# Kernel optimization log

Hardware: AMD Instinct MI355X
Metric: run time of the kernel (lower is better)

## Reference

```python
import jax, jax.numpy as jnp
import numpy as np

N, E, B, F, TLEN, NVOC, EMB, EPS = 131072, 1048576, 512, 78, 1000, 26, 128, 1e-5


def setup_inputs() -> dict:
    key = jax.random.key(0)
    ks = jax.random.split(key, 64)
    it = iter(range(64))

    def nrm(shp, s=0.05):
        return jax.random.normal(ks[next(it)], shp, jnp.float32) * s

    def bnp(c):  # row 0 = gamma, row 1 = beta (eval-mode BN, running stats = 0/1)
        return jnp.stack([1.0 + nrm((c,)), nrm((c,))])

    inp = {
        "x": jax.random.normal(ks[next(it)], (N, F), jnp.float32),
        "edge_index": jax.random.randint(ks[next(it)], (2, E), 0, N),
        "batch": jnp.repeat(jnp.arange(B), N // B),  # sorted graph ids, 256 nodes/graph
        "target": jax.random.randint(ks[next(it)], (B, TLEN), 0, NVOC),
        "W1": nrm((F, F)), "b1": nrm((F,)), "bn1": bnp(F), "Wp1": nrm((F, 1)), "bp1": nrm((1,)),
        "W2": nrm((F, F)), "b2": nrm((F,)), "bn2": bnp(F), "Wp2": nrm((F, 1)), "bp2": nrm((1,)),
        "W3": nrm((F, F)), "b3": nrm((F,)), "bn3": bnp(F), "Wp3": nrm((F, 1)), "bp3": nrm((1,)),
        "fcg1_W": nrm((2 * F, 128)), "fcg1_b": nrm((128,)), "bn4": bnp(128),
        "emb": nrm((NVOC, EMB), 1.0),
        "c1W": nrm((128, TLEN, 3)), "c1b": nrm((128,)), "bnx1": bnp(128),
        "c2W": nrm((64, 128, 3)), "c2b": nrm((64,)), "bnx2": bnp(64),
        "c3W": nrm((32, 64, 3)), "c3b": nrm((32,)), "bnx3": bnp(32),
        "fxt_W": nrm((32 * 128, 128)), "fxt_b": nrm((128,)), "bn6": bnp(128),
        "fc1W": nrm((256, 1024)), "fc1b": nrm((1024,)), "bn7": bnp(1024),
        "fc2W": nrm((1024, 512)), "fc2b": nrm((512,)), "bn8": bnp(512),
        "outW": nrm((512, 1)), "outb": nrm((1,)),
    }
    return inp


def _bn(h, p, axis=1):
    # eval-mode BatchNorm with running_mean=0, running_var=1
    sh = [1] * h.ndim
    sh[axis] = -1
    return h * (p[0] / jnp.sqrt(1.0 + EPS)).reshape(sh) + p[1].reshape(sh)


def reference(x, edge_index, batch, target, W1, b1, bn1, Wp1, bp1, W2, b2, bn2, Wp2, bp2,
              W3, b3, bn3, Wp3, bp3, fcg1_W, fcg1_b, bn4, emb, c1W, c1b, bnx1, c2W, c2b,
              bnx2, c3W, c3b, bnx3, fxt_W, fxt_b, bn6, fc1W, fc1b, bn7, fc2W, fc2b, bn8,
              outW, outb):
    src, dst = edge_index[0], edge_index[1]
    n = x.shape[0]

    # GCNConv with added self-loops and symmetric normalization
    deg = jax.ops.segment_sum(jnp.ones(src.shape[0], x.dtype), dst, num_segments=n) + 1.0
    dis = jax.lax.rsqrt(deg)                       # deg^{-1/2} including self-loop
    coef = (dis[src] * dis[dst])[:, None]          # [E,1]
    selfc = (dis * dis)[:, None]                   # [N,1]

    def gcn(h, W, b):
        h = h @ W
        agg = jax.ops.segment_sum(h[src] * coef, dst, num_segments=n)
        return agg + h * selfc + b

    def readout(h):
        mx = jax.ops.segment_max(h, batch, num_segments=B)
        cnt = jax.ops.segment_sum(jnp.ones(n, h.dtype), batch, num_segments=B)
        mean = jax.ops.segment_sum(h, batch, num_segments=B) / cnt[:, None]
        return jnp.concatenate([mx, mean], axis=1)  # [B, 2F]

    def block(h, W, b, bnp, Wp, bp):
        h = jax.nn.relu(_bn(gcn(h, W, b), bnp))
        # SAGPooling with ratio=1.0 keeps every node: x <- x * tanh(score)
        s = gcn(h, Wp, bp)[:, 0]
        return h * jnp.tanh(s)[:, None]

    h = block(x, W1, b1, bn1, Wp1, bp1); x1 = readout(h)
    h = block(h, W2, b2, bn2, Wp2, bp2); x2 = readout(h)
    h = block(h, W3, b3, bn3, Wp3, bp3); x3 = readout(h)
    g = jax.nn.relu(_bn((x1 + x2 + x3) @ fcg1_W + fcg1_b, bn4))

    # protein branch: embed [B,1000,128], conv1d over embed axis with 1000 in-channels
    def conv1d(h, W, b):
        o = jax.lax.conv_general_dilated(h, W, (1,), ((1, 1),),
                                         dimension_numbers=("NCH", "OIH", "NCH"))
        return o + b[None, :, None]

    e = emb[target]                                # [B, 1000, 128]
    p = jax.nn.relu(_bn(conv1d(e, c1W, c1b), bnx1))
    p = jax.nn.relu(_bn(conv1d(p, c2W, c2b), bnx2))
    p = jax.nn.relu(_bn(conv1d(p, c3W, c3b), bnx3))  # [B, 32, 128]
    xt = _bn(jax.nn.relu(p.reshape(p.shape[0], -1) @ fxt_W + fxt_b), bn6)

    xc = jnp.concatenate([g, xt], axis=1)          # [B, 256]
    xc = _bn(jax.nn.relu(xc @ fc1W + fc1b), bn7)
    xc = _bn(jax.nn.relu(xc @ fc2W + fc2b), bn8)
    return xc @ outW + outb
```

## Files before the change

kernel.cpp:

```cpp
#include <hip/hip_runtime.h>
#include <hip/hip_bf16.h>
#include <cstddef>

#define N_NODES 131072
#define N_EDGES 1048576
#define NF 78
#define NB 512
#define BNR 0.9999950000374996f

typedef float v2f __attribute__((ext_vector_type(2)));

__device__ __forceinline__ float wave_red_sum(float v) {
  for (int off = 32; off > 0; off >>= 1) v += __shfl_down(v, off);
  return v;
}

__device__ __forceinline__ float bf2f(unsigned short u) {
  return __uint_as_float(((unsigned)u) << 16);
}

__device__ __forceinline__ unsigned f2bf_rn(float x) {
  unsigned u = __float_as_uint(x);
  return (u + 0x7fffu + ((u >> 16) & 1u)) >> 16;
}

__device__ __forceinline__ unsigned char f2fp8(float x) {
  int p = __builtin_amdgcn_cvt_pk_fp8_f32(x, x, 0, false);
  return (unsigned char)(p & 0xff);
}

__global__ void k_count(const int* __restrict__ dst, int* __restrict__ cnt) {
  int e = blockIdx.x * 256 + threadIdx.x;
  if (e < N_EDGES) atomicAdd(&cnt[dst[e]], 1);
}

__global__ void k_dis(const int* __restrict__ cnt, float* __restrict__ dis) {
  int n = blockIdx.x * 256 + threadIdx.x;
  if (n < N_NODES) dis[n] = rsqrtf(1.0f + (float)cnt[n]);
}

__global__ void k_scan1(const int* __restrict__ cnt, int* __restrict__ offs, int* __restrict__ bsum) {
  __shared__ int s[512];
  int gid = blockIdx.x * 512 + threadIdx.x;
  int v = cnt[gid];
  s[threadIdx.x] = v; __syncthreads();
  for (int off = 1; off < 512; off <<= 1) {
    int t = (threadIdx.x >= off) ? s[threadIdx.x - off] : 0;
    __syncthreads();
    s[threadIdx.x] += t;
    __syncthreads();
  }
  offs[gid] = s[threadIdx.x] - v;
  if (threadIdx.x == 511) bsum[blockIdx.x] = s[511];
}

__global__ void k_scan2(int* __restrict__ bsum) {
  __shared__ int s[256];
  int v = bsum[threadIdx.x];
  s[threadIdx.x] = v; __syncthreads();
  for (int off = 1; off < 256; off <<= 1) {
    int t = (threadIdx.x >= off) ? s[threadIdx.x - off] : 0;
    __syncthreads();
    s[threadIdx.x] += t;
    __syncthreads();
  }
  bsum[threadIdx.x] = s[threadIdx.x] - v;
}

__global__ void k_scan3(int* __restrict__ offs, const int* __restrict__ bsum) {
  int gid = blockIdx.x * 512 + threadIdx.x;
  offs[gid] += bsum[blockIdx.x];
}

__global__ void k_fill(const int* __restrict__ src, const int* __restrict__ dst,
                       const int* __restrict__ offs, int* __restrict__ cursor,
                       const float* __restrict__ dis, int* __restrict__ csr,
                       float* __restrict__ cf) {
  int e = blockIdx.x * 256 + threadIdx.x;
  if (e < N_EDGES) {
    int s = src[e], d = dst[e];
    int pos = offs[d] + atomicAdd(&cursor[d], 1);
    csr[pos] = s;
    cf[pos] = dis[s] * dis[d];
  }
}

__global__ __launch_bounds__(256) void k_gemm_f32(const float* __restrict__ h,
                                                  const float* __restrict__ W,
                                                  unsigned char* __restrict__ t8) {
  __shared__ float hs[64 * NF];
  __shared__ float Ws[NF * NF];
  int n0 = blockIdx.x * 64;
  int tid = threadIdx.x;
  for (int i = tid; i < NF * NF; i += 256) Ws[i] = W[i];
  for (int i = tid; i < 64 * NF; i += 256) hs[i] = h[(size_t)n0 * NF + i];
  __syncthreads();
  int rg = tid >> 4, cg = tid & 15;
  int r0 = rg * 4, c0 = cg * 5;
  float acc[4][5] = {};
  for (int k = 0; k < NF; ++k) {
    float wv[5];
#pragma unroll
    for (int j = 0; j < 5; ++j) wv[j] = (c0 + j < NF) ? Ws[k * NF + c0 + j] : 0.f;
#pragma unroll
    for (int i = 0; i < 4; ++i) {
      float hv = hs[(r0 + i) * NF + k];
#pragma unroll
      for (int j = 0; j < 5; ++j) acc[i][j] += hv * wv[j];
    }
  }
  for (int i = 0; i < 4; ++i)
    for (int j = 0; j < 5; ++j) {
      int c = c0 + j;
      if (c < NF) t8[(size_t)(n0 + r0 + i) * 128 + c] = f2fp8(acc[i][j]);
    }
}

__global__ __launch_bounds__(256) void k_gemm_bf16(const unsigned short* __restrict__ h,
                                                   const float* __restrict__ gate,
                                                   const float* __restrict__ W,
                                                   unsigned char* __restrict__ t8) {
  __shared__ float hs[64 * NF];
  __shared__ float Ws[NF * NF];
  int n0 = blockIdx.x * 64;
  int tid = threadIdx.x;
  for (int i = tid; i < NF * NF; i += 256) Ws[i] = W[i];
  for (int i = tid; i < 64 * NF; i += 256) {
    int r = i / NF;
    hs[i] = bf2f(h[(size_t)n0 * NF + i]) * gate[n0 + r];
  }
  __syncthreads();
  int rg = tid >> 4, cg = tid & 15;
  int r0 = rg * 4, c0 = cg * 5;
  float acc[4][5] = {};
  for (int k = 0; k < NF; ++k) {
    float wv[5];
#pragma unroll
    for (int j = 0; j < 5; ++j) wv[j] = (c0 + j < NF) ? Ws[k * NF + c0 + j] : 0.f;
#pragma unroll
    for (int i = 0; i < 4; ++i) {
      float hv = hs[(r0 + i) * NF + k];
#pragma unroll
      for (int j = 0; j < 5; ++j) acc[i][j] += hv * wv[j];
    }
  }
  for (int i = 0; i < 4; ++i)
    for (int j = 0; j < 5; ++j) {
      int c = c0 + j;
      if (c < NF) t8[(size_t)(n0 + r0 + i) * 128 + c] = f2fp8(acc[i][j]);
    }
}

__global__ __launch_bounds__(256) void k_agg(const unsigned short* __restrict__ t16, const int* __restrict__ offs,
                                             const int* __restrict__ cnt, const int* __restrict__ csr,
                                             const float* __restrict__ cf, const float* __restrict__ dis,
                                             const float* __restrict__ bias, const float* __restrict__ bn,
                                             const float* __restrict__ Wp,
                                             unsigned* __restrict__ hout, float* __restrict__ spre) {
  int wave = threadIdx.x >> 6, lane = threadIdx.x & 63;
  int n = blockIdx.x * 4 + wave;
  float disn = dis[n];
  int st = offs[n], cn = cnt[n];
  int cn1 = cn < 64 ? cn : 64;
  int sIdx = 0; float sCoef = 0.f;
  if (lane < cn1) {
    sIdx = csr[st + lane] * 64;
    sCoef = cf[st + lane];
  }
  int lc = lane < 39 ? lane : 38;
  float selfc = disn * disn;
  unsigned su = t16[(size_t)n * 64 + lc];
  v2f sf = __builtin_amdgcn_cvt_pk_f32_fp8(su, false);
  float a0e = sf[0] * selfc;
  float a1e = sf[1] * selfc;
  float a0o = 0.f, a1o = 0.f;
  int j = 0;
#pragma unroll 4
  for (; j + 2 <= cn1; j += 2) {
    int sb0 = __shfl(sIdx, j);     float c0 = __shfl(sCoef, j);
    int sb1 = __shfl(sIdx, j + 1); float c1 = __shfl(sCoef, j + 1);
    unsigned u0 = t16[sb0 + lc];
    unsigned u1 = t16[sb1 + lc];
    v2f f0 = __builtin_amdgcn_cvt_pk_f32_fp8(u0, false);
    v2f f1 = __builtin_amdgcn_cvt_pk_f32_fp8(u1, false);
    a0e += c0 * f0[0];
    a1e += c0 * f0[1];
    a0o += c1 * f1[0];
    a1o += c1 * f1[1];
  }
  if (j < cn1) {
    int sb = __shfl(sIdx, j); float c = __shfl(sCoef, j);
    unsigned u = t16[sb + lc];
    v2f f = __builtin_amdgcn_cvt_pk_f32_fp8(u, false);
    a0e += c * f[0];
    a1e += c * f[1];
  }
  for (j = 64; j < cn; ++j) {
    int sb = csr[st + j] * 64; float c = cf[st + j];
    unsigned u = t16[sb + lc];
    v2f f = __builtin_amdgcn_cvt_pk_f32_fp8(u, false);
    a0e += c * f[0];
    a1e += c * f[1];
  }
  float a0 = a0e + a0o, a1 = a1e + a1o;
  float h0 = 0.f, h1 = 0.f;
  float2 wp = make_float2(0.f, 0.f);
  if (lane < 39) {
    float2 bi = *reinterpret_cast<const float2*>(bias + 2 * lane);
    float2 gm = *reinterpret_cast<const float2*>(bn + 2 * lane);
    float2 bt = *reinterpret_cast<const float2*>(bn + NF + 2 * lane);
    h0 = fmaxf(0.f, gm.x * BNR * (a0 + bi.x) + bt.x);
    h1 = fmaxf(0.f, gm.y * BNR * (a1 + bi.y) + bt.y);
    hout[(size_t)n * 39 + lane] = f2bf_rn(h0) | (f2bf_rn(h1) << 16);
    wp = *reinterpret_cast<const float2*>(Wp + 2 * lane);
  }
  float p = h0 * wp.x + h1 * wp.y;
  p = wave_red_sum(p);
  if (lane == 0) spre[n] = p;
}

__global__ void k_gate(const float* __restrict__ spre, const int* __restrict__ offs,
                       const int* __restrict__ cnt, const int* __restrict__ csr,
                       const float* __restrict__ cf, const float* __restrict__ dis,
                       const float* __restrict__ bp, float* __restrict__ gate) {
  int n = blockIdx.x * 256 + threadIdx.x;
  if (n >= N_NODES) return;
  float disn = dis[n];
  float s = bp[0] + disn * disn * spre[n];
  int st = offs[n], cn = cnt[n];
#pragma unroll 4
  for (int j = 0; j < cn; ++j) {
    s += cf[st + j] * spre[csr[st + j]];
  }
  gate[n] = tanhf(s);
}

__global__ __launch_bounds__(128) void k_readout(const unsigned short* __restrict__ h,
                                                 const float* __restrict__ gate,
                                                 float* __restrict__ xsum, int accum) {
  __shared__ float gl[256];
  int b = blockIdx.x, tid = threadIdx.x;
  for (int i = tid; i < 256; i += 128) gl[i] = gate[b * 256 + i];
  __syncthreads();
  if (tid >= NF) return;
  float mx = -1e30f, sm = 0.f;
  const unsigned short* hp = h + (size_t)b * 256 * NF + tid;
  for (int nn = 0; nn < 256; ++nn) {
    float v = bf2f(hp[(size_t)nn * NF]) * gl[nn];
    mx = fmaxf(mx, v);
    sm += v;
  }
  float mean = sm * (1.f / 256.f);
  if (accum) {
    xsum[b * 156 + tid] += mx;
    xsum[b * 156 + NF + tid] += mean;
  } else {
    xsum[b * 156 + tid] = mx;
    xsum[b * 156 + NF + tid] = mean;
  }
}

__global__ __launch_bounds__(128) void k_fcg(const float* __restrict__ xsum, const float* __restrict__ W,
                                             const float* __restrict__ bias, const float* __restrict__ bn,
                                             float* __restrict__ g) {
  __shared__ float xs[156];
  int b = blockIdx.x, tid = threadIdx.x;
  for (int i = tid; i < 156; i += 128) xs[i] = xsum[b * 156 + i];
  __syncthreads();
  float acc = bias[tid];
  for (int i = 0; i < 156; ++i) acc += xs[i] * W[i * 128 + tid];
  g[b * 128 + tid] = fmaxf(0.f, bn[tid] * BNR * acc + bn[128 + tid]);
}

__global__ void k_transpose_w(const float* __restrict__ c1W, float* __restrict__ Wt) {
  int idx = blockIdx.x * 256 + threadIdx.x;
  if (idx >= 384000) return;
  int i = idx / 384;
  int r = idx - i * 384;
  int oc = r / 3, k = r - oc * 3;
  Wt[idx] = c1W[oc * 3000 + i * 3 + k];
}

__global__ __launch_bounds__(512) void k_conv1(const float* __restrict__ Wt, const int* __restrict__ target,
                                               const float* __restrict__ emb, const float* __restrict__ c1b,
                                               const float* __restrict__ bnx, float* __restrict__ O) {
  __shared__ float G[26 * 384];
  __shared__ float el[26 * 132];
  __shared__ int tg[1000];
  __shared__ int border[1000];
  __shared__ int cnt26[26], boff[27], cur26[26];
  int b = blockIdx.x, tid = threadIdx.x;
  if (tid < 26) cnt26[tid] = 0;
  for (int i = tid; i < 26 * 132; i += 512) {
    int v = i / 132, hp = i - v * 132;
    el[i] = (hp >= 1 && hp <= 128) ? emb[v * 128 + hp - 1] : 0.f;
  }
  for (int i = tid; i < 1000; i += 512) tg[i] = target[b * 1000 + i];
  __syncthreads();
  for (int i = tid; i < 1000; i += 512) atomicAdd(&cnt26[tg[i]], 1);
  __syncthreads();
  if (tid == 0) {
    int run = 0;
    for (int v = 0; v < 26; ++v) { boff[v] = run; cur26[v] = run; run += cnt26[v]; }
    boff[26] = run;
  }
  __syncthreads();
  for (int i = tid; i < 1000; i += 512) {
    int v = tg[i];
    int slot = atomicAdd(&cur26[v], 1);
    border[slot] = i;
  }
  __syncthreads();
  if (tid < 384) {
    for (int v = 0; v < 26; ++v) {
      int k0 = boff[v], k1 = boff[v + 1];
      float ae = 0.f, ao = 0.f;
      int k = k0;
#pragma unroll 4
      for (; k + 2 <= k1; k += 2) {
        int p0 = border[k];
        int p1 = border[k + 1];
        ae += Wt[(size_t)p0 * 384 + tid];
        ao += Wt[(size_t)p1 * 384 + tid];
      }
      if (k < k1) ae += Wt[(size_t)border[k] * 384 + tid];
      G[v * 384 + tid] = ae + ao;
    }
  }
  __syncthreads();
  int oc = tid & 127, q = tid >> 7;
  int h0 = q * 32;
  float acc[32];
#pragma unroll
  for (int j = 0; j < 32; ++j) acc[j] = 0.f;
  for (int v = 0; v < 26; ++v) {
    float g0 = G[v * 384 + oc * 3 + 0];
    float g1 = G[v * 384 + oc * 3 + 1];
    float g2 = G[v * 384 + oc * 3 + 2];
    float4 buf[9];
    const float4* ep = reinterpret_cast<const float4*>(&el[v * 132 + h0]);
#pragma unroll
    for (int r = 0; r < 9; ++r) buf[r] = ep[r];
    const float* bf = reinterpret_cast<const float*>(buf);
#pragma unroll
    for (int j = 0; j < 32; ++j)
      acc[j] += g0 * bf[j] + g1 * bf[j + 1] + g2 * bf[j + 2];
  }
  float bia = c1b[oc];
  float sc = bnx[oc] * BNR, bt = bnx[128 + oc];
  float* outp = O + (size_t)b * 16384 + oc * 128 + h0;
#pragma unroll
  for (int j = 0; j < 32; ++j) acc[j] = fmaxf(0.f, sc * (acc[j] + bia) + bt);
#pragma unroll
  for (int j = 0; j < 8; ++j)
    *reinterpret_cast<float4*>(outp + 4 * j) =
        make_float4(acc[4 * j], acc[4 * j + 1], acc[4 * j + 2], acc[4 * j + 3]);
}

__global__ __launch_bounds__(256) void k_conv2(const float* __restrict__ X, const float* __restrict__ W,
                                               const float* __restrict__ bias, const float* __restrict__ bnx,
                                               float* __restrict__ O) {
  __shared__ float xl[128 * 136];
  int b = blockIdx.x, tid = threadIdx.x;
  for (int i = tid; i < 128 * 32; i += 256) {
    int row = i >> 5, c4 = (i & 31) * 4;
    float4 v = *reinterpret_cast<const float4*>(X + (size_t)b * 16384 + row * 128 + c4);
    *reinterpret_cast<float4*>(&xl[row * 136 + 4 + c4]) = v;
  }
  if (tid < 128) { xl[tid * 136 + 3] = 0.f; xl[tid * 136 + 132] = 0.f; }
  __syncthreads();
  int oc = tid & 63, q = tid >> 6;
  int h0 = q * 32;
  float acc[32];
#pragma unroll
  for (int j = 0; j < 32; ++j) acc[j] = 0.f;
  const float* wp = W + oc * 384;
  for (int i = 0; i < 128; ++i) {
    float w0 = wp[i * 3], w1 = wp[i * 3 + 1], w2 = wp[i * 3 + 2];
    float4 buf[10];
    const float4* xp = reinterpret_cast<const float4*>(&xl[i * 136 + h0]);
#pragma unroll
    for (int r = 0; r < 10; ++r) buf[r] = xp[r];
    const float* bf = reinterpret_cast<const float*>(buf);
#pragma unroll
    for (int j = 0; j < 32; ++j)
      acc[j] += w0 * bf[3 + j] + w1 * bf[4 + j] + w2 * bf[5 + j];
  }
  float bia = bias[oc], sc = bnx[oc] * BNR, bt = bnx[64 + oc];
  float* outp = O + (size_t)b * 8192 + oc * 128 + h0;
#pragma unroll
  for (int j = 0; j < 32; ++j) acc[j] = fmaxf(0.f, sc * (acc[j] + bia) + bt);
#pragma unroll
  for (int j = 0; j < 8; ++j)
    *reinterpret_cast<float4*>(outp + 4 * j) =
        make_float4(acc[4 * j], acc[4 * j + 1], acc[4 * j + 2], acc[4 * j + 3]);
}

__global__ __launch_bounds__(256) void k_conv3(const float* __restrict__ X, const float* __restrict__ W,
                                               const float* __restrict__ bias, const float* __restrict__ bnx,
                                               float* __restrict__ O) {
  __shared__ float xl[64 * 136];
  int b = blockIdx.x, tid = threadIdx.x;
  for (int i = tid; i < 64 * 32; i += 256) {
    int row = i >> 5, c4 = (i & 31) * 4;
    float4 v = *reinterpret_cast<const float4*>(X + (size_t)b * 8192 + row * 128 + c4);
    *reinterpret_cast<float4*>(&xl[row * 136 + 4 + c4]) = v;
  }
  if (tid < 64) { xl[tid * 136 + 3] = 0.f; xl[tid * 136 + 132] = 0.f; }
  __syncthreads();
  int oc = tid & 31, q = tid >> 5;
  int h0 = q * 16;
  float acc[16];
#pragma unroll
  for (int j = 0; j < 16; ++j) acc[j] = 0.f;
  const float* wp = W + oc * 192;
  for (int i = 0; i < 64; ++i) {
    float w0 = wp[i * 3], w1 = wp[i * 3 + 1], w2 = wp[i * 3 + 2];
    float4 buf[6];
    const float4* xp = reinterpret_cast<const float4*>(&xl[i * 136 + h0]);
#pragma unroll
    for (int r = 0; r < 6; ++r) buf[r] = xp[r];
    const float* bf = reinterpret_cast<const float*>(buf);
#pragma unroll
    for (int j = 0; j < 16; ++j)
      acc[j] += w0 * bf[3 + j] + w1 * bf[4 + j] + w2 * bf[5 + j];
  }
  float bia = bias[oc], sc = bnx[oc] * BNR, bt = bnx[32 + oc];
  float* outp = O + (size_t)b * 4096 + oc * 128 + h0;
#pragma unroll
  for (int j = 0; j < 16; ++j) acc[j] = fmaxf(0.f, sc * (acc[j] + bia) + bt);
#pragma unroll
  for (int j = 0; j < 4; ++j)
    *reinterpret_cast<float4*>(outp + 4 * j) =
        make_float4(acc[4 * j], acc[4 * j + 1], acc[4 * j + 2], acc[4 * j + 3]);
}

__global__ __launch_bounds__(128) void k_fxt_part(const float* __restrict__ P, const float* __restrict__ W,
                                                  float* __restrict__ part) {
  __shared__ float pl[8 * 512];
  int bblk = blockIdx.x >> 3, kc = blockIdx.x & 7;
  int b0 = bblk * 8, tid = threadIdx.x;
  for (int i = tid; i < 8 * 512; i += 128) {
    int bb = i >> 9, k = i & 511;
    pl[i] = P[(size_t)(b0 + bb) * 4096 + kc * 512 + k];
  }
  __syncthreads();
  float acc[8] = {};
  const float* wp = W + (size_t)kc * 512 * 128 + tid;
  for (int k = 0; k < 512; ++k) {
    float w = wp[(size_t)k * 128];
#pragma unroll
    for (int bb = 0; bb < 8; ++bb) acc[bb] += pl[bb * 512 + k] * w;
  }
#pragma unroll
  for (int bb = 0; bb < 8; ++bb)
    part[((size_t)kc * 512 + b0 + bb) * 128 + tid] = acc[bb];
}

__global__ __launch_bounds__(256) void k_fxt_red(const float* __restrict__ part, const float* __restrict__ bias,
                                                 const float* __restrict__ bn, float* __restrict__ xt) {
  int idx = blockIdx.x * 256 + threadIdx.x;
  int j = idx & 127;
  float s = 0.f;
#pragma unroll
  for (int kc = 0; kc < 8; ++kc) s += part[(size_t)kc * 65536 + idx];
  xt[idx] = bn[j] * BNR * fmaxf(0.f, s + bias[j]) + bn[128 + j];
}

__global__ __launch_bounds__(256) void k_fc1(const float* __restrict__ g, const float* __restrict__ xt,
                                             const float* __restrict__ W, const float* __restrict__ bias,
                                             const float* __restrict__ bn, float* __restrict__ out) {
  __shared__ float al[4 * 256];
  int bblk = blockIdx.x >> 2, jb = blockIdx.x & 3;
  int b0 = bblk * 4, tid = threadIdx.x;
  int j = jb * 256 + tid;
  for (int i = tid; i < 4 * 256; i += 256) {
    int bb = i >> 8, c = i & 255;
    al[i] = (c < 128) ? g[(b0 + bb) * 128 + c] : xt[(b0 + bb) * 128 + c - 128];
  }
  __syncthreads();
  float acc[4] = {};
  for (int i = 0; i < 256; ++i) {
    float w = W[(size_t)i * 1024 + j];
#pragma unroll
    for (int bb = 0; bb < 4; ++bb) acc[bb] += al[bb * 256 + i] * w;
  }
  float bi = bias[j], sc = bn[j] * BNR, bt = bn[1024 + j];
#pragma unroll
  for (int bb = 0; bb < 4; ++bb)
    out[(size_t)(b0 + bb) * 1024 + j] = sc * fmaxf(0.f, acc[bb] + bi) + bt;
}

__global__ __launch_bounds__(256) void k_fc2(const float* __restrict__ xc1, const float* __restrict__ W,
                                             const float* __restrict__ bias, const float* __restrict__ bn,
                                             float* __restrict__ out) {
  __shared__ float al[4 * 1024];
  int bblk = blockIdx.x >> 1, jb = blockIdx.x & 1;
  int b0 = bblk * 4, tid = threadIdx.x;
  int j = jb * 256 + tid;
  for (int i = tid; i < 4 * 1024; i += 256)
    al[i] = xc1[(size_t)(b0 + (i >> 10)) * 1024 + (i & 1023)];
  __syncthreads();
  float acc[4] = {};
  for (int i = 0; i < 1024; ++i) {
    float w = W[(size_t)i * 512 + j];
#pragma unroll
    for (int bb = 0; bb < 4; ++bb) acc[bb] += al[bb * 1024 + i] * w;
  }
  float bi = bias[j], sc = bn[j] * BNR, bt = bn[512 + j];
#pragma unroll
  for (int bb = 0; bb < 4; ++bb)
    out[(size_t)(b0 + bb) * 512 + j] = sc * fmaxf(0.f, acc[bb] + bi) + bt;
}

__global__ __launch_bounds__(256) void k_out(const float* __restrict__ xc2, const float* __restrict__ W,
                                             const float* __restrict__ ob, float* __restrict__ out) {
  __shared__ float red[4];
  int b = blockIdx.x, tid = threadIdx.x;
  float v = xc2[(size_t)b * 512 + tid] * W[tid] + xc2[(size_t)b * 512 + 256 + tid] * W[256 + tid];
  v = wave_red_sum(v);
  int wave = tid >> 6, lane = tid & 63;
  if (lane == 0) red[wave] = v;
  __syncthreads();
  if (tid == 0) out[b] = red[0] + red[1] + red[2] + red[3] + ob[0];
}

extern "C" void kernel_launch(void* const* d_in, const int* in_sizes, int n_in,
                              void* d_out, int out_size, void* d_ws, size_t ws_size,
                              hipStream_t stream) {
  (void)in_sizes; (void)n_in; (void)out_size; (void)ws_size;
  const float* x      = (const float*)d_in[0];
  const int*   eidx   = (const int*)d_in[1];
  const int*   src    = eidx;
  const int*   dst    = eidx + N_EDGES;
  const int*   target = (const int*)d_in[3];
  const float* W1 = (const float*)d_in[4];  const float* b1 = (const float*)d_in[5];
  const float* bn1 = (const float*)d_in[6]; const float* Wp1 = (const float*)d_in[7];
  const float* bp1 = (const float*)d_in[8];
  const float* W2 = (const float*)d_in[9];  const float* b2 = (const float*)d_in[10];
  const float* bn2 = (const float*)d_in[11]; const float* Wp2 = (const float*)d_in[12];
  const float* bp2 = (const float*)d_in[13];
  const float* W3 = (const float*)d_in[14]; const float* b3 = (const float*)d_in[15];
  const float* bn3 = (const float*)d_in[16]; const float* Wp3 = (const float*)d_in[17];
  const float* bp3 = (const float*)d_in[18];
  const float* fcg1_W = (const float*)d_in[19]; const float* fcg1_b = (const float*)d_in[20];
  const float* bn4 = (const float*)d_in[21];
  const float* emb = (const float*)d_in[22];
  const float* c1W = (const float*)d_in[23]; const float* c1b = (const float*)d_in[24];
  const float* bnx1 = (const float*)d_in[25];
  const float* c2W = (const float*)d_in[26]; const float* c2b = (const float*)d_in[27];
  const float* bnx2 = (const float*)d_in[28];
  const float* c3W = (const float*)d_in[29]; const float* c3b = (const float*)d_in[30];
  const float* bnx3 = (const float*)d_in[31];
  const float* fxt_W = (const float*)d_in[32]; const float* fxt_b = (const float*)d_in[33];
  const float* bn6 = (const float*)d_in[34];
  const float* fc1W = (const float*)d_in[35]; const float* fc1b = (const float*)d_in[36];
  const float* bn7 = (const float*)d_in[37];
  const float* fc2W = (const float*)d_in[38]; const float* fc2b = (const float*)d_in[39];
  const float* bn8 = (const float*)d_in[40];
  const float* outW = (const float*)d_in[41]; const float* outb = (const float*)d_in[42];

  char* ws = (char*)d_ws;
  size_t off = 0;
  auto alloc = [&](size_t bytes) -> void* {
    void* p = ws + off;
    off += (bytes + 255) & ~(size_t)255;
    return p;
  };
  float* dis   = (float*)alloc((size_t)N_NODES * 4);
  int*   cnt   = (int*)alloc((size_t)N_NODES * 4);
  int*   cursor= (int*)alloc((size_t)N_NODES * 4);
  int*   offs  = (int*)alloc((size_t)N_NODES * 4);
  int*   bsum  = (int*)alloc(1024);
  int*   csr   = (int*)alloc((size_t)N_EDGES * 4);
  float* cf    = (float*)alloc((size_t)N_EDGES * 4);
  float* h_a   = (float*)alloc((size_t)N_NODES * NF * 4);
  float* h_b   = (float*)alloc((size_t)N_NODES * NF * 4);
  float* tbuf  = (float*)alloc((size_t)N_NODES * NF * 4);
  float* gate  = (float*)alloc((size_t)N_NODES * 4);
  float* spre  = (float*)alloc((size_t)N_NODES * 4);
  float* xsum  = (float*)alloc(512 * 156 * 4);
  float* gbuf  = (float*)alloc(512 * 128 * 4);
  float* xt    = (float*)alloc(512 * 128 * 4);
  float* xc1   = (float*)alloc(512 * 1024 * 4);
  float* xc2   = (float*)alloc(512 * 512 * 4);
  unsigned char*  t8  = (unsigned char*)tbuf;
  unsigned short* t16 = (unsigned short*)tbuf;
  unsigned* ha_u = (unsigned*)h_a;  unsigned short* ha_s = (unsigned short*)h_a;
  unsigned* hb_u = (unsigned*)h_b;  unsigned short* hb_s = (unsigned short*)h_b;
  float* O1 = h_a;
  float* O2 = h_b;
  float* Wt = tbuf;
  float* P  = tbuf + 5242880;
  float* fxt_part = h_a;

  hipMemsetAsync(cnt, 0, (size_t)N_NODES * 4, stream);
  hipMemsetAsync(cursor, 0, (size_t)N_NODES * 4, stream);

  k_count<<<N_EDGES / 256, 256, 0, stream>>>(dst, cnt);
  k_dis<<<N_NODES / 256, 256, 0, stream>>>(cnt, dis);
  k_scan1<<<N_NODES / 512, 512, 0, stream>>>(cnt, offs, bsum);
  k_scan2<<<1, 256, 0, stream>>>(bsum);
  k_scan3<<<N_NODES / 512, 512, 0, stream>>>(offs, bsum);
  k_fill<<<N_EDGES / 256, 256, 0, stream>>>(src, dst, offs, cursor, dis, csr, cf);

  k_gemm_f32<<<N_NODES / 64, 256, 0, stream>>>(x, W1, t8);
  k_agg<<<N_NODES / 4, 256, 0, stream>>>(t16, offs, cnt, csr, cf, dis, b1, bn1, Wp1, ha_u, spre);
  k_gate<<<N_NODES / 256, 256, 0, stream>>>(spre, offs, cnt, csr, cf, dis, bp1, gate);
  k_readout<<<NB, 128, 0, stream>>>(ha_s, gate, xsum, 0);
  k_gemm_bf16<<<N_NODES / 64, 256, 0, stream>>>(ha_s, gate, W2, t8);
  k_agg<<<N_NODES / 4, 256, 0, stream>>>(t16, offs, cnt, csr, cf, dis, b2, bn2, Wp2, hb_u, spre);
  k_gate<<<N_NODES / 256, 256, 0, stream>>>(spre, offs, cnt, csr, cf, dis, bp2, gate);
  k_readout<<<NB, 128, 0, stream>>>(hb_s, gate, xsum, 1);
  k_gemm_bf16<<<N_NODES / 64, 256, 0, stream>>>(hb_s, gate, W3, t8);
  k_agg<<<N_NODES / 4, 256, 0, stream>>>(t16, offs, cnt, csr, cf, dis, b3, bn3, Wp3, ha_u, spre);
  k_gate<<<N_NODES / 256, 256, 0, stream>>>(spre, offs, cnt, csr, cf, dis, bp3, gate);
  k_readout<<<NB, 128, 0, stream>>>(ha_s, gate, xsum, 1);

  k_fcg<<<NB, 128, 0, stream>>>(xsum, fcg1_W, fcg1_b, bn4, gbuf);

  k_transpose_w<<<1500, 256, 0, stream>>>(c1W, Wt);
  k_conv1<<<NB, 512, 0, stream>>>(Wt, target, emb, c1b, bnx1, O1);
  k_conv2<<<NB, 256, 0, stream>>>(O1, c2W, c2b, bnx2, O2);
  k_conv3<<<NB, 256, 0, stream>>>(O2, c3W, c3b, bnx3, P);
  k_fxt_part<<<512, 128, 0, stream>>>(P, fxt_W, fxt_part);
  k_fxt_red<<<256, 256, 0, stream>>>(fxt_part, fxt_b, bn6, xt);

  k_fc1<<<512, 256, 0, stream>>>(gbuf, xt, fc1W, fc1b, bn7, xc1);
  k_fc2<<<256, 256, 0, stream>>>(xc1, fc2W, fc2b, bn8, xc2);
  k_out<<<NB, 256, 0, stream>>>(xc2, outW, outb, (float*)d_out);
}
```

Baseline: 752.5 us.

## Split agg wave into three neighbor slots and halve conv2 per-block work with bf16 LDS

k_agg now has each lane read 4 fp8 features per 32-bit load, so 20 lanes cover a row. A wave therefore processes three neighbors at once, with indices staged in LDS and the partial sums combined by shuffles. This cuts the number of serial gather iterations per node. Separately, conv2 is split across two blocks per batch item (32 output channels each) and stores the input tile in LDS as bf16. That doubles the grid, reduces registers per thread and halves LDS, at the cost of an extra rounding of conv2's inputs.

```diff
diff --git a/kernel.cpp b/kernel.cpp
--- a/kernel.cpp
+++ b/kernel.cpp
@@ -151,70 +151,92 @@
     }
 }
 
-__global__ __launch_bounds__(256) void k_agg(const unsigned short* __restrict__ t16, const int* __restrict__ offs,
+__global__ __launch_bounds__(256) void k_agg(const unsigned* __restrict__ t32, const int* __restrict__ offs,
                                              const int* __restrict__ cnt, const int* __restrict__ csr,
                                              const float* __restrict__ cf, const float* __restrict__ dis,
                                              const float* __restrict__ bias, const float* __restrict__ bn,
                                              const float* __restrict__ Wp,
                                              unsigned* __restrict__ hout, float* __restrict__ spre) {
+  __shared__ int   sIdxL[4 * 68];
+  __shared__ float sCoefL[4 * 68];
   int wave = threadIdx.x >> 6, lane = threadIdx.x & 63;
   int n = blockIdx.x * 4 + wave;
   float disn = dis[n];
   int st = offs[n], cn = cnt[n];
   int cn1 = cn < 64 ? cn : 64;
-  int sIdx = 0; float sCoef = 0.f;
+  int base = wave * 68;
   if (lane < cn1) {
-    sIdx = csr[st + lane] * 64;
-    sCoef = cf[st + lane];
-  }
-  int lc = lane < 39 ? lane : 38;
+    int s = csr[st + lane];
+    sIdxL[base + lane] = s * 32;
+    sCoefL[base + lane] = cf[st + lane];
+  }
+  if (lane < 3) {
+    sIdxL[base + cn1 + lane] = 0;
+    sCoefL[base + cn1 + lane] = 0.f;
+  }
+  int slot = lane / 20;
+  int li = lane - slot * 20;
   float selfc = disn * disn;
-  unsigned su = t16[(size_t)n * 64 + lc];
-  v2f sf = __builtin_amdgcn_cvt_pk_f32_fp8(su, false);
-  float a0e = sf[0] * selfc;
-  float a1e = sf[1] * selfc;
-  float a0o = 0.f, a1o = 0.f;
-  int j = 0;
-#pragma unroll 4
-  for (; j + 2 <= cn1; j += 2) {
-    int sb0 = __shfl(sIdx, j);     float c0 = __shfl(sCoef, j);
-    int sb1 = __shfl(sIdx, j + 1); float c1 = __shfl(sCoef, j + 1);
-    unsigned u0 = t16[sb0 + lc];
-    unsigned u1 = t16[sb1 + lc];
-    v2f f0 = __builtin_amdgcn_cvt_pk_f32_fp8(u0, false);
-    v2f f1 = __builtin_amdgcn_cvt_pk_f32_fp8(u1, false);
-    a0e += c0 * f0[0];
-    a1e += c0 * f0[1];
-    a0o += c1 * f1[0];
-    a1o += c1 * f1[1];
-  }
-  if (j < cn1) {
-    int sb = __shfl(sIdx, j); float c = __shfl(sCoef, j);
-    unsigned u = t16[sb + lc];
-    v2f f = __builtin_amdgcn_cvt_pk_f32_fp8(u, false);
-    a0e += c * f[0];
-    a1e += c * f[1];
-  }
-  for (j = 64; j < cn; ++j) {
-    int sb = csr[st + j] * 64; float c = cf[st + j];
-    unsigned u = t16[sb + lc];
-    v2f f = __builtin_amdgcn_cvt_pk_f32_fp8(u, false);
-    a0e += c * f[0];
-    a1e += c * f[1];
-  }
-  float a0 = a0e + a0o, a1 = a1e + a1o;
-  float h0 = 0.f, h1 = 0.f;
-  float2 wp = make_float2(0.f, 0.f);
-  if (lane < 39) {
-    float2 bi = *reinterpret_cast<const float2*>(bias + 2 * lane);
-    float2 gm = *reinterpret_cast<const float2*>(bn + 2 * lane);
-    float2 bt = *reinterpret_cast<const float2*>(bn + NF + 2 * lane);
-    h0 = fmaxf(0.f, gm.x * BNR * (a0 + bi.x) + bt.x);
-    h1 = fmaxf(0.f, gm.y * BNR * (a1 + bi.y) + bt.y);
-    hout[(size_t)n * 39 + lane] = f2bf_rn(h0) | (f2bf_rn(h1) << 16);
-    wp = *reinterpret_cast<const float2*>(Wp + 2 * lane);
-  }
-  float p = h0 * wp.x + h1 * wp.y;
+  float a0 = 0.f, a1 = 0.f, a2 = 0.f, a3 = 0.f;
+  if (slot == 0) {
+    unsigned u = t32[(size_t)n * 32 + li];
+    v2f f01 = __builtin_amdgcn_cvt_pk_f32_fp8((int)u, false);
+    v2f f23 = __builtin_amdgcn_cvt_pk_f32_fp8((int)u, true);
+    a0 = f01[0] * selfc; a1 = f01[1] * selfc;
+    a2 = f23[0] * selfc; a3 = f23[1] * selfc;
+  }
+#pragma unroll 2
+  for (int j = 0; j < cn1; j += 3) {
+    int idx = sIdxL[base + j + slot];
+    float c = (slot < 3) ? sCoefL[base + j + slot] : 0.f;
+    unsigned u = t32[idx + li];
+    v2f f01 = __builtin_amdgcn_cvt_pk_f32_fp8((int)u, false);
+    v2f f23 = __builtin_amdgcn_cvt_pk_f32_fp8((int)u, true);
+    a0 += c * f01[0]; a1 += c * f01[1];
+    a2 += c * f23[0]; a3 += c * f23[1];
+  }
+  for (int j = 64; j < cn; ++j) {
+    if (slot == 0) {
+      int sb = csr[st + j] * 32; float c = cf[st + j];
+      unsigned u = t32[sb + li];
+      v2f f01 = __builtin_amdgcn_cvt_pk_f32_fp8((int)u, false);
+      v2f f23 = __builtin_amdgcn_cvt_pk_f32_fp8((int)u, true);
+      a0 += c * f01[0]; a1 += c * f01[1];
+      a2 += c * f23[0]; a3 += c * f23[1];
+    }
+  }
+  a0 += __shfl(a0, lane + 20) + __shfl(a0, lane + 40);
+  a1 += __shfl(a1, lane + 20) + __shfl(a1, lane + 40);
+  a2 += __shfl(a2, lane + 20) + __shfl(a2, lane + 40);
+  a3 += __shfl(a3, lane + 20) + __shfl(a3, lane + 40);
+  float p = 0.f;
+  if (lane < 20) {
+    int f0 = 4 * lane;
+    float h0v, h1v, h2v, h3v;
+    if (lane < 19) {
+      float4 bi = *reinterpret_cast<const float4*>(bias + f0);
+      float4 gm = *reinterpret_cast<const float4*>(bn + f0);
+      float2 btA = *reinterpret_cast<const float2*>(bn + NF + f0);
+      float2 btB = *reinterpret_cast<const float2*>(bn + NF + f0 + 2);
+      float4 wp = *reinterpret_cast<const float4*>(Wp + f0);
+      h0v = fmaxf(0.f, gm.x * BNR * (a0 + bi.x) + btA.x);
+      h1v = fmaxf(0.f, gm.y * BNR * (a1 + bi.y) + btA.y);
+      h2v = fmaxf(0.f, gm.z * BNR * (a2 + bi.z) + btB.x);
+      h3v = fmaxf(0.f, gm.w * BNR * (a3 + bi.w) + btB.y);
+      hout[(size_t)n * 39 + 2 * lane]     = f2bf_rn(h0v) | (f2bf_rn(h1v) << 16);
+      hout[(size_t)n * 39 + 2 * lane + 1] = f2bf_rn(h2v) | (f2bf_rn(h3v) << 16);
+      p = h0v * wp.x + h1v * wp.y + h2v * wp.z + h3v * wp.w;
+    } else {
+      float2 bi = *reinterpret_cast<const float2*>(bias + 76);
+      float2 gm = *reinterpret_cast<const float2*>(bn + 76);
+      float2 bt = *reinterpret_cast<const float2*>(bn + NF + 76);
+      float2 wp = *reinterpret_cast<const float2*>(Wp + 76);
+      h0v = fmaxf(0.f, gm.x * BNR * (a0 + bi.x) + bt.x);
+      h1v = fmaxf(0.f, gm.y * BNR * (a1 + bi.y) + bt.y);
+      hout[(size_t)n * 39 + 38] = f2bf_rn(h0v) | (f2bf_rn(h1v) << 16);
+      p = h0v * wp.x + h1v * wp.y;
+    }
+  }
   p = wave_red_sum(p);
   if (lane == 0) spre[n] = p;
 }
@@ -360,38 +382,45 @@
 __global__ __launch_bounds__(256) void k_conv2(const float* __restrict__ X, const float* __restrict__ W,
                                                const float* __restrict__ bias, const float* __restrict__ bnx,
                                                float* __restrict__ O) {
-  __shared__ float xl[128 * 136];
-  int b = blockIdx.x, tid = threadIdx.x;
-  for (int i = tid; i < 128 * 32; i += 256) {
-    int row = i >> 5, c4 = (i & 31) * 4;
-    float4 v = *reinterpret_cast<const float4*>(X + (size_t)b * 16384 + row * 128 + c4);
-    *reinterpret_cast<float4*>(&xl[row * 136 + 4 + c4]) = v;
-  }
-  if (tid < 128) { xl[tid * 136 + 3] = 0.f; xl[tid * 136 + 132] = 0.f; }
-  __syncthreads();
-  int oc = tid & 63, q = tid >> 6;
-  int h0 = q * 32;
-  float acc[32];
-#pragma unroll
-  for (int j = 0; j < 32; ++j) acc[j] = 0.f;
+  __shared__ unsigned xl[128 * 68];
+  int bid = blockIdx.x;
+  int b = bid >> 1, og = bid & 1;
+  int tid = threadIdx.x;
+  for (int t = tid; t < 4096; t += 256) {
+    int r = t >> 5, c = t & 31;
+    float4 v = *reinterpret_cast<const float4*>(X + (size_t)b * 16384 + r * 128 + 4 * c);
+    xl[r * 68 + 2 * c + 2] = f2bf_rn(v.x) | (f2bf_rn(v.y) << 16);
+    xl[r * 68 + 2 * c + 3] = f2bf_rn(v.z) | (f2bf_rn(v.w) << 16);
+  }
+  if (tid < 128) { xl[tid * 68 + 1] = 0u; xl[tid * 68 + 66] = 0u; }
+  __syncthreads();
+  int oc = og * 32 + (tid & 31), q = tid >> 5;
+  float acc[16];
+#pragma unroll
+  for (int j = 0; j < 16; ++j) acc[j] = 0.f;
   const float* wp = W + oc * 384;
   for (int i = 0; i < 128; ++i) {
     float w0 = wp[i * 3], w1 = wp[i * 3 + 1], w2 = wp[i * 3 + 2];
-    float4 buf[10];
-    const float4* xp = reinterpret_cast<const float4*>(&xl[i * 136 + h0]);
-#pragma unroll
-    for (int r = 0; r < 10; ++r) buf[r] = xp[r];
-    const float* bf = reinterpret_cast<const float*>(buf);
-#pragma unroll
-    for (int j = 0; j < 32; ++j)
+    uint4 ub[3];
+    const uint4* xp = reinterpret_cast<const uint4*>(&xl[i * 68 + 8 * q]);
+    ub[0] = xp[0]; ub[1] = xp[1]; ub[2] = xp[2];
+    const unsigned* uu = reinterpret_cast<const unsigned*>(ub);
+    float bf[24];
+#pragma unroll
+    for (int d = 0; d < 12; ++d) {
+      bf[2 * d]     = __uint_as_float(uu[d] << 16);
+      bf[2 * d + 1] = __uint_as_float(uu[d] & 0xffff0000u);
+    }
+#pragma unroll
+    for (int j = 0; j < 16; ++j)
       acc[j] += w0 * bf[3 + j] + w1 * bf[4 + j] + w2 * bf[5 + j];
   }
   float bia = bias[oc], sc = bnx[oc] * BNR, bt = bnx[64 + oc];
-  float* outp = O + (size_t)b * 8192 + oc * 128 + h0;
-#pragma unroll
-  for (int j = 0; j < 32; ++j) acc[j] = fmaxf(0.f, sc * (acc[j] + bia) + bt);
-#pragma unroll
-  for (int j = 0; j < 8; ++j)
+  float* outp = O + (size_t)b * 8192 + oc * 128 + 16 * q;
+#pragma unroll
+  for (int j = 0; j < 16; ++j) acc[j] = fmaxf(0.f, sc * (acc[j] + bia) + bt);
+#pragma unroll
+  for (int j = 0; j < 4; ++j)
     *reinterpret_cast<float4*>(outp + 4 * j) =
         make_float4(acc[4 * j], acc[4 * j + 1], acc[4 * j + 2], acc[4 * j + 3]);
 }
@@ -585,7 +614,7 @@
   float* xc1   = (float*)alloc(512 * 1024 * 4);
   float* xc2   = (float*)alloc(512 * 512 * 4);
   unsigned char*  t8  = (unsigned char*)tbuf;
-  unsigned short* t16 = (unsigned short*)tbuf;
+  unsigned*       tu  = (unsigned*)tbuf;
   unsigned* ha_u = (unsigned*)h_a;  unsigned short* ha_s = (unsigned short*)h_a;
   unsigned* hb_u = (unsigned*)h_b;  unsigned short* hb_s = (unsigned short*)h_b;
   float* O1 = h_a;
@@ -605,15 +634,15 @@
   k_fill<<<N_EDGES / 256, 256, 0, stream>>>(src, dst, offs, cursor, dis, csr, cf);
 
   k_gemm_f32<<<N_NODES / 64, 256, 0, stream>>>(x, W1, t8);
-  k_agg<<<N_NODES / 4, 256, 0, stream>>>(t16, offs, cnt, csr, cf, dis, b1, bn1, Wp1, ha_u, spre);
+  k_agg<<<N_NODES / 4, 256, 0, stream>>>(tu, offs, cnt, csr, cf, dis, b1, bn1, Wp1, ha_u, spre);
   k_gate<<<N_NODES / 256, 256, 0, stream>>>(spre, offs, cnt, csr, cf, dis, bp1, gate);
   k_readout<<<NB, 128, 0, stream>>>(ha_s, gate, xsum, 0);
   k_gemm_bf16<<<N_NODES / 64, 256, 0, stream>>>(ha_s, gate, W2, t8);
-  k_agg<<<N_NODES / 4, 256, 0, stream>>>(t16, offs, cnt, csr, cf, dis, b2, bn2, Wp2, hb_u, spre);
+  k_agg<<<N_NODES / 4, 256, 0, stream>>>(tu, offs, cnt, csr, cf, dis, b2, bn2, Wp2, hb_u, spre);
   k_gate<<<N_NODES / 256, 256, 0, stream>>>(spre, offs, cnt, csr, cf, dis, bp2, gate);
   k_readout<<<NB, 128, 0, stream>>>(hb_s, gate, xsum, 1);
   k_gemm_bf16<<<N_NODES / 64, 256, 0, stream>>>(hb_s, gate, W3, t8);
-  k_agg<<<N_NODES / 4, 256, 0, stream>>>(t16, offs, cnt, csr, cf, dis, b3, bn3, Wp3, ha_u, spre);
+  k_agg<<<N_NODES / 4, 256, 0, stream>>>(tu, offs, cnt, csr, cf, dis, b3, bn3, Wp3, ha_u, spre);
   k_gate<<<N_NODES / 256, 256, 0, stream>>>(spre, offs, cnt, csr, cf, dis, bp3, gate);
   k_readout<<<NB, 128, 0, stream>>>(ha_s, gate, xsum, 1);
 
@@ -621,7 +650,7 @@
 
   k_transpose_w<<<1500, 256, 0, stream>>>(c1W, Wt);
   k_conv1<<<NB, 512, 0, stream>>>(Wt, target, emb, c1b, bnx1, O1);
-  k_conv2<<<NB, 256, 0, stream>>>(O1, c2W, c2b, bnx2, O2);
+  k_conv2<<<NB * 2, 256, 0, stream>>>(O1, c2W, c2b, bnx2, O2);
   k_conv3<<<NB, 256, 0, stream>>>(O2, c3W, c3b, bnx3, P);
   k_fxt_part<<<512, 128, 0, stream>>>(P, fxt_W, fxt_part);
   k_fxt_red<<<256, 256, 0, stream>>>(fxt_part, fxt_b, bn6, xt);
```

Result: no change. 754.6 us (+0.3%).
